# Optimization experiments

Hardware: AMD Instinct MI355X
Metric: run time of the kernel (lower is better)

The kernel has to match this reference:

```python
import jax, jax.numpy as jnp
import numpy as np

N_HEADS = 16
HEAD_DIM = 128


def _rotate_half(x):
    x1, x2 = jnp.split(x, 2, axis=-1)
    return jnp.concatenate((-x2, x1), axis=-1)


def setup_inputs() -> dict:
    key = jax.random.key(0)
    ks = jax.random.split(key, 6)
    B, T, D = 2, 2048, 2048
    d = D // N_HEADS  # 128
    x = jax.random.normal(ks[0], (B, T, D), dtype=jnp.float32)
    # RoPE tables (shape [1,1,T,head_dim]) built as in standard implementations
    inv_freq = 1.0 / (10000.0 ** (jnp.arange(0, d, 2, dtype=jnp.float32) / d))
    ang = jnp.arange(T, dtype=jnp.float32)[:, None] * inv_freq[None, :]  # [T, d/2]
    emb = jnp.concatenate((ang, ang), axis=-1)  # [T, d]
    rope_cos = jnp.cos(emb)[None, None]
    rope_sin = jnp.sin(emb)[None, None]
    qkv_w = jax.random.normal(ks[1], (3 * D, D), dtype=jnp.float32) * (1.0 / np.sqrt(D))
    qkv_b = jnp.zeros((3 * D,), dtype=jnp.float32)
    out_w = jax.random.normal(ks[2], (D, D), dtype=jnp.float32) * (1.0 / np.sqrt(D))
    out_b = jnp.zeros((D,), dtype=jnp.float32)
    return {"x": x, "rope_cos": rope_cos, "rope_sin": rope_sin,
            "qkv_w": qkv_w, "qkv_b": qkv_b, "out_w": out_w, "out_b": out_b}


def reference(x, rope_cos, rope_sin, qkv_w, qkv_b, out_w, out_b):
    B, T, D = x.shape
    H, d = N_HEADS, D // N_HEADS
    # fused QKV projection: [B,T,3D] -> [3,B,H,T,d]
    qkv = (jnp.einsum('btd,ed->bte', x, qkv_w) + qkv_b)
    qkv = qkv.reshape(B, T, 3, H, d).transpose(2, 0, 3, 1, 4)
    q, k, v = qkv[0], qkv[1], qkv[2]
    cos = rope_cos[:, :, :T, :].astype(q.dtype)
    sin = rope_sin[:, :, :T, :].astype(q.dtype)
    q = q * cos + _rotate_half(q) * sin
    k = k * cos + _rotate_half(k) * sin
    # causal SDPA
    scale = 1.0 / jnp.sqrt(jnp.array(d, dtype=q.dtype))
    scores = jnp.einsum('bhqd,bhkd->bhqk', q, k) * scale  # [B,H,T,T]
    causal = jnp.tril(jnp.ones((T, T), dtype=bool))
    scores = jnp.where(causal, scores, jnp.finfo(scores.dtype).min)
    attn = jax.nn.softmax(scores, axis=-1)
    out = jnp.einsum('bhqk,bhkd->bhqd', attn, v)  # [B,H,T,d]
    out = out.transpose(0, 2, 1, 3).reshape(B, T, D)
    return jnp.einsum('btd,ed->bte', out, out_w) + out_b
```

## Files before the change

kernel.cpp:

```cpp
#include <hip/hip_runtime.h>
#include <cstdint>
#include <cstddef>

typedef unsigned short u16;
using bf16x8 = __attribute__((ext_vector_type(8))) short;
using f32x4  = __attribute__((ext_vector_type(4))) float;

#define MFMA16(a, b, c) __builtin_amdgcn_mfma_f32_16x16x32_bf16((a), (b), (c), 0, 0, 0)

__device__ __forceinline__ u16 f2bf(float f) {
  union { float f; unsigned u; } x; x.f = f;
  unsigned r = x.u + 0x7fffu + ((x.u >> 16) & 1u);
  return (u16)(r >> 16);
}
__device__ __forceinline__ float bf2f(u16 h) {
  union { unsigned u; float f; } x; x.u = ((unsigned)h) << 16;
  return x.f;
}
__device__ __forceinline__ void gll16(const void* g, void* l) {
  __builtin_amdgcn_global_load_lds((const __attribute__((address_space(1))) void*)g,
                                   (__attribute__((address_space(3))) void*)l, 16, 0, 0);
}

union U8 { bf16x8 v; u16 u[8]; };

__global__ __launch_bounds__(256) void cvt_kernel(const float* __restrict__ in,
                                                  u16* __restrict__ out, int n4) {
  int i = blockIdx.x * blockDim.x + threadIdx.x;
  if (i >= n4) return;
  float4 v = ((const float4*)in)[i];
  ushort4 o;
  o.x = f2bf(v.x); o.y = f2bf(v.y); o.z = f2bf(v.z); o.w = f2bf(v.w);
  ((ushort4*)out)[i] = o;
}

__global__ __launch_bounds__(512, 2) void gemm_bt256(const u16* __restrict__ A,
                                                     const u16* __restrict__ Bw,
                                                     const float* __restrict__ bias,
                                                     void* __restrict__ Cout,
                                                     int M, int N, int K, int out_bf16) {
  __shared__ u16 As_[2][16384];
  __shared__ u16 Bs_[2][16384];
  const int tid = threadIdx.x;
  const int lane = tid & 63, wave = tid >> 6;
  const int col = lane & 15, quad = lane >> 4;
  const int wr = wave >> 2, wc = wave & 3;
  const int bm = blockIdx.y, bn = blockIdx.x;
  const u16* Ag = A + (size_t)bm * 256 * K;
  const u16* Bg = Bw + (size_t)bn * 256 * K;
  const int srow = tid >> 2;
  const int sslot = tid & 3;
  const int ssw = (sslot ^ ((srow >> 1) & 3)) << 3;
  const size_t g0 = (size_t)srow * K + ssw;
  const size_t g1 = (size_t)(srow + 128) * K + ssw;
  const int swq = (quad ^ ((col >> 1) & 3)) << 3;
  const int aro = (wr * 128 + col) * 32 + swq;
  const int bro = (wc * 64 + col) * 32 + swq;
  u16* const As0 = &As_[0][0]; u16* const As1 = &As_[1][0];
  u16* const Bs0 = &Bs_[0][0]; u16* const Bs1 = &Bs_[1][0];
  f32x4 acc[8][4] = {};
  bf16x8 a[8], bq[2];
  const int NI = K >> 7;

#define STG_A(BUF, KS, KT) do { \
    gll16(Ag + g0 + (KT) + (KS) * 32, (void*)((BUF) + (KS) * 8192 + tid * 8)); \
    gll16(Ag + g1 + (KT) + (KS) * 32, (void*)((BUF) + (KS) * 8192 + 4096 + tid * 8)); } while (0)
#define STG_B(BUF, KS, KT) do { \
    gll16(Bg + g0 + (KT) + (KS) * 32, (void*)((BUF) + (KS) * 8192 + tid * 8)); \
    gll16(Bg + g1 + (KT) + (KS) * 32, (void*)((BUF) + (KS) * 8192 + 4096 + tid * 8)); } while (0)
#define RD_A(BUF, KS) do { _Pragma("unroll") \
    for (int m_ = 0; m_ < 8; m_++) \
      a[m_] = *(const bf16x8*)&(BUF)[(KS) * 8192 + aro + m_ * 512]; } while (0)
#define RD_B(BUF, KS, NH) do { _Pragma("unroll") \
    for (int n_ = 0; n_ < 2; n_++) \
      bq[n_] = *(const bf16x8*)&(BUF)[(KS) * 8192 + bro + ((NH) * 2 + n_) * 512]; } while (0)
#define MM(NH) do { _Pragma("unroll") \
    for (int m_ = 0; m_ < 8; m_++) { _Pragma("unroll") \
      for (int n_ = 0; n_ < 2; n_++) \
        acc[m_][(NH) * 2 + n_] = MFMA16(a[m_], bq[n_], acc[m_][(NH) * 2 + n_]); } } while (0)
#define PH(RDS, STGS, MMS, WT) do { \
    RDS; STGS; \
    __builtin_amdgcn_s_barrier(); \
    asm volatile("s_waitcnt lgkmcnt(0)" ::: "memory"); \
    __builtin_amdgcn_s_setprio(1); \
    MMS; \
    __builtin_amdgcn_s_setprio(0); \
    WT; \
    __builtin_amdgcn_s_barrier(); } while (0)
#define VM6 do { asm volatile("s_waitcnt vmcnt(6)" ::: "memory"); } while (0)
#define VM0 do { asm volatile("s_waitcnt vmcnt(0)" ::: "memory"); } while (0)
#define NOPW do { } while (0)

#define ITER(I, LAST) do { \
    const int kt1_ = ((2 * (I) + 1) << 6), kt2_ = kt1_ + 64, kt3_ = kt2_ + 64; \
    PH({ RD_A(As0, 0); RD_B(Bs0, 0, 0); }, { STG_B(Bs1, 1, kt1_); },                MM(0), NOPW); \
    PH({ RD_B(Bs0, 0, 1); },               { if (!(LAST)) STG_A(As0, 0, kt2_); },   MM(1), NOPW); \
    PH({ RD_A(As0, 1); RD_B(Bs0, 1, 1); }, { if (!(LAST)) STG_B(Bs0, 0, kt2_); },   MM(1), NOPW); \
    PH({ RD_B(Bs0, 1, 0); },               { if (!(LAST)) STG_A(As0, 1, kt2_); },   MM(0), \
       if (LAST) { VM0; } else { VM6; }); \
    PH({ RD_A(As1, 0); RD_B(Bs1, 0, 0); }, { if (!(LAST)) STG_B(Bs0, 1, kt2_); },   MM(0), NOPW); \
    PH({ RD_B(Bs1, 0, 1); },               { if (!(LAST)) STG_A(As1, 0, kt3_); },   MM(1), NOPW); \
    PH({ RD_A(As1, 1); RD_B(Bs1, 1, 1); }, { if (!(LAST)) STG_B(Bs1, 0, kt3_); },   MM(1), NOPW); \
    PH({ RD_B(Bs1, 1, 0); },               { if (!(LAST)) STG_A(As1, 1, kt3_); },   MM(0), \
       if (!(LAST)) { VM6; }); \
  } while (0)

  STG_A(As0, 0, 0);  STG_B(Bs0, 0, 0);  STG_A(As0, 1, 0);  STG_B(Bs0, 1, 0);
  STG_A(As1, 0, 64); STG_B(Bs1, 0, 64); STG_A(As1, 1, 64);
  VM6;
  __builtin_amdgcn_s_barrier();

  for (int i = 0; i < NI - 1; ++i) ITER(i, false);
  ITER(NI - 1, true);

#pragma unroll
  for (int i = 0; i < 8; i++) {
    const int row0 = bm * 256 + wr * 128 + i * 16 + quad * 4;
#pragma unroll
    for (int j = 0; j < 4; j++) {
      const int cn = bn * 256 + wc * 64 + j * 16 + col;
      const float bv = bias[cn];
#pragma unroll
      for (int r = 0; r < 4; r++) {
        float v = acc[i][j][r] + bv;
        size_t off = (size_t)(row0 + r) * N + cn;
        if (out_bf16) ((u16*)Cout)[off] = f2bf(v);
        else          ((float*)Cout)[off] = v;
      }
    }
  }
#undef STG_A
#undef STG_B
#undef RD_A
#undef RD_B
#undef MM
#undef PH
#undef VM6
#undef VM0
#undef NOPW
#undef ITER
}

__global__ __launch_bounds__(256) void rope_kernel(const u16* __restrict__ qkv,
                                                   const float* __restrict__ cosT,
                                                   const float* __restrict__ sinT,
                                                   u16* __restrict__ qo,
                                                   u16* __restrict__ ko,
                                                   u16* __restrict__ vt) {
  __shared__ u16 vs[128 * 72];
  const int bh = blockIdx.x;
  const int b = bh >> 4, h = bh & 15;
  const int tb = blockIdx.y;
  const int tid = threadIdx.x;
  const int tl = tid >> 2;
  const int g = tid & 3;
  const int t = tb * 64 + tl;
  const size_t qrow = ((size_t)(b * 2048 + t)) * 6144 + h * 128;
  const size_t orow = ((size_t)bh * 2048 + t) * 128;
  const int tt = t * 128;
  const int dl = g * 16, dh = 64 + dl;
  const float scale = 0.08838834764831845f;
#pragma unroll
  for (int cch = 0; cch < 2; cch++) {
    const int o8 = cch * 8;
    U8 ql, qh, kl, kh, vl, vh;
    ql.v = *(const bf16x8*)&qkv[qrow + dl + o8];
    qh.v = *(const bf16x8*)&qkv[qrow + dh + o8];
    kl.v = *(const bf16x8*)&qkv[qrow + 2048 + dl + o8];
    kh.v = *(const bf16x8*)&qkv[qrow + 2048 + dh + o8];
    vl.v = *(const bf16x8*)&qkv[qrow + 4096 + dl + o8];
    vh.v = *(const bf16x8*)&qkv[qrow + 4096 + dh + o8];
    float cl[8], ch_[8], sl[8], sh_[8];
    *(float4*)&cl[0]  = *(const float4*)&cosT[tt + dl + o8];
    *(float4*)&cl[4]  = *(const float4*)&cosT[tt + dl + o8 + 4];
    *(float4*)&ch_[0] = *(const float4*)&cosT[tt + dh + o8];
    *(float4*)&ch_[4] = *(const float4*)&cosT[tt + dh + o8 + 4];
    *(float4*)&sl[0]  = *(const float4*)&sinT[tt + dl + o8];
    *(float4*)&sl[4]  = *(const float4*)&sinT[tt + dl + o8 + 4];
    *(float4*)&sh_[0] = *(const float4*)&sinT[tt + dh + o8];
    *(float4*)&sh_[4] = *(const float4*)&sinT[tt + dh + o8 + 4];
    U8 aq, bq, ak, bk;
#pragma unroll
    for (int i = 0; i < 8; i++) {
      float qlf = bf2f(ql.u[i]), qhf = bf2f(qh.u[i]);
      float klf = bf2f(kl.u[i]), khf = bf2f(kh.u[i]);
      aq.u[i] = f2bf((qlf * cl[i]  - qhf * sl[i])  * scale);
      bq.u[i] = f2bf((qhf * ch_[i] + qlf * sh_[i]) * scale);
      ak.u[i] = f2bf(klf * cl[i]  - khf * sl[i]);
      bk.u[i] = f2bf(khf * ch_[i] + klf * sh_[i]);
    }
    *(bf16x8*)&qo[orow + dl + o8] = aq.v;
    *(bf16x8*)&qo[orow + dh + o8] = bq.v;
    *(bf16x8*)&ko[orow + dl + o8] = ak.v;
    *(bf16x8*)&ko[orow + dh + o8] = bk.v;
#pragma unroll
    for (int i = 0; i < 8; i++) {
      vs[(dl + o8 + i) * 72 + tl] = vl.u[i];
      vs[(dh + o8 + i) * 72 + tl] = vh.u[i];
    }
  }
  __syncthreads();
#pragma unroll
  for (int c = 0; c < 4; c++) {
    int idx = c * 256 + tid;
    int dd = idx >> 3, chk = idx & 7;
    bf16x8 vv = *(const bf16x8*)&vs[dd * 72 + chk * 8];
    *(bf16x8*)&vt[((size_t)bh * 128 + dd) * 2048 + tb * 64 + chk * 8] = vv;
  }
}

__global__ __launch_bounds__(256) void attn_kernel(const u16* __restrict__ Q,
                                                   const u16* __restrict__ Kk,
                                                   const u16* __restrict__ Vt,
                                                   u16* __restrict__ O) {
  __shared__ u16 Ks[64 * 136];
  __shared__ u16 Vs[128 * 72];
  __shared__ u16 Ps[4][16 * 72];
  const int bh = blockIdx.y, b = bh >> 4, h = bh & 15;
  const int qtile = gridDim.x - 1 - blockIdx.x;
  const int qb = qtile * 128;
  const int tid = threadIdx.x, wave = tid >> 6, lane = tid & 63;
  const int col = lane & 15, quad = lane >> 4;
  const int qw0 = qb + wave * 32;
  const int qw1 = qw0 + 16;
  const u16* Qg = Q + (size_t)bh * 2048 * 128;
  const u16* Kg = Kk + (size_t)bh * 2048 * 128;
  const u16* Vg = Vt + (size_t)bh * 128 * 2048;
  bf16x8 qf0[4], qf1[4];
#pragma unroll
  for (int c = 0; c < 4; c++) {
    qf0[c] = *(const bf16x8*)&Qg[(size_t)(qw0 + col) * 128 + c * 32 + quad * 8];
    qf1[c] = *(const bf16x8*)&Qg[(size_t)(qw1 + col) * 128 + c * 32 + quad * 8];
  }
  f32x4 o0[8] = {}, o1[8] = {};
  float ls0[4] = {0.f, 0.f, 0.f, 0.f}, ls1[4] = {0.f, 0.f, 0.f, 0.f};
  const int ntiles = (qb + 128) >> 6;
  const int kr = tid >> 2, kc = (tid & 3) * 8;
  const int vr = tid >> 1, vc = (tid & 1) * 8;
  for (int it = 0; it < ntiles; ++it) {
    const int kt = it << 6;
    __syncthreads();
#pragma unroll
    for (int u = 0; u < 4; u++)
      *(bf16x8*)&Ks[kr * 136 + kc + u * 32] =
          *(const bf16x8*)&Kg[(size_t)(kt + kr) * 128 + kc + u * 32];
#pragma unroll
    for (int u = 0; u < 4; u++)
      *(bf16x8*)&Vs[vr * 72 + vc + u * 16] =
          *(const bf16x8*)&Vg[(size_t)vr * 2048 + kt + vc + u * 16];
    __syncthreads();
    if (kt > qw1 + 15) continue;
    const bool do0 = (kt <= qw0 + 15);
    f32x4 s0[4] = {}, s1[4] = {};
#pragma unroll
    for (int c = 0; c < 4; c++) {
#pragma unroll
      for (int kg = 0; kg < 4; kg++) {
        bf16x8 kf = *(const bf16x8*)&Ks[(kg * 16 + col) * 136 + c * 32 + quad * 8];
        s0[kg] = MFMA16(qf0[c], kf, s0[kg]);
        s1[kg] = MFMA16(qf1[c], kf, s1[kg]);
      }
    }
    u16* pw = Ps[wave];
    if (do0) {
#pragma unroll
      for (int kg = 0; kg < 4; kg++)
#pragma unroll
        for (int r = 0; r < 4; r++) {
          int key = kt + kg * 16 + col, qg = qw0 + quad * 4 + r;
          float p = (key <= qg) ? __expf(s0[kg][r]) : 0.f;
          ls0[r] += p;
          pw[(quad * 4 + r) * 72 + kg * 16 + col] = f2bf(p);
        }
#pragma unroll
      for (int ks = 0; ks < 64; ks += 32) {
        bf16x8 pf = *(const bf16x8*)&pw[col * 72 + ks + quad * 8];
#pragma unroll
        for (int dt = 0; dt < 8; dt++) {
          bf16x8 vf = *(const bf16x8*)&Vs[(dt * 16 + col) * 72 + ks + quad * 8];
          o0[dt] = MFMA16(pf, vf, o0[dt]);
        }
      }
    }
    {
#pragma unroll
      for (int kg = 0; kg < 4; kg++)
#pragma unroll
        for (int r = 0; r < 4; r++) {
          int key = kt + kg * 16 + col, qg = qw1 + quad * 4 + r;
          float p = (key <= qg) ? __expf(s1[kg][r]) : 0.f;
          ls1[r] += p;
          pw[(quad * 4 + r) * 72 + kg * 16 + col] = f2bf(p);
        }
#pragma unroll
      for (int ks = 0; ks < 64; ks += 32) {
        bf16x8 pf = *(const bf16x8*)&pw[col * 72 + ks + quad * 8];
#pragma unroll
        for (int dt = 0; dt < 8; dt++) {
          bf16x8 vf = *(const bf16x8*)&Vs[(dt * 16 + col) * 72 + ks + quad * 8];
          o1[dt] = MFMA16(pf, vf, o1[dt]);
        }
      }
    }
  }
#pragma unroll
  for (int st = 1; st < 16; st <<= 1)
#pragma unroll
    for (int r = 0; r < 4; r++) {
      ls0[r] += __shfl_xor(ls0[r], st);
      ls1[r] += __shfl_xor(ls1[r], st);
    }
#pragma unroll
  for (int r = 0; r < 4; r++) {
    float inv0 = 1.0f / ls0[r], inv1 = 1.0f / ls1[r];
    size_t row0 = ((size_t)(b * 2048 + qw0 + quad * 4 + r)) * 2048 + h * 128;
    size_t row1 = ((size_t)(b * 2048 + qw1 + quad * 4 + r)) * 2048 + h * 128;
#pragma unroll
    for (int dt = 0; dt < 8; dt++) {
      O[row0 + dt * 16 + col] = f2bf(o0[dt][r] * inv0);
      O[row1 + dt * 16 + col] = f2bf(o1[dt][r] * inv1);
    }
  }
}

extern "C" void kernel_launch(void* const* d_in, const int* in_sizes, int n_in,
                              void* d_out, int out_size, void* d_ws, size_t ws_size,
                              hipStream_t stream) {
  const float* x        = (const float*)d_in[0];
  const float* rope_cos = (const float*)d_in[1];
  const float* rope_sin = (const float*)d_in[2];
  const float* qkv_w    = (const float*)d_in[3];
  const float* qkv_b    = (const float*)d_in[4];
  const float* out_w    = (const float*)d_in[5];
  const float* out_b    = (const float*)d_in[6];
  float* out = (float*)d_out;
  u16* ws = (u16*)d_ws;
  u16* xb    = ws;
  u16* wqkvb = xb + 8388608;
  u16* woutb = wqkvb + 12582912;
  u16* qkvb  = woutb + 4194304;
  u16* qb    = qkvb + 25165824;
  u16* kb    = qb + 8388608;
  u16* vtb   = kb + 8388608;
  u16* attnb = xb;

  cvt_kernel<<<8192, 256, 0, stream>>>(x, xb, 2097152);
  cvt_kernel<<<12288, 256, 0, stream>>>(qkv_w, wqkvb, 3145728);
  cvt_kernel<<<4096, 256, 0, stream>>>(out_w, woutb, 1048576);
  gemm_bt256<<<dim3(24, 16), 512, 0, stream>>>(xb, wqkvb, qkv_b, qkvb, 4096, 6144, 2048, 1);
  rope_kernel<<<dim3(32, 32), 256, 0, stream>>>(qkvb, rope_cos, rope_sin, qb, kb, vtb);
  attn_kernel<<<dim3(16, 32), 256, 0, stream>>>(qb, kb, vtb, attnb);
  gemm_bt256<<<dim3(8, 16), 512, 0, stream>>>(attnb, woutb, out_b, out, 4096, 2048, 2048, 0);
}
```

Baseline: 452.4 us.

## Add triple-buffered NT GEMM for output projection and swizzle attention LDS tiles

Adds a templated gemm_nt kernel with a 256x128 tile, triple-buffered global-to-LDS loads, split MFMA phases with priority hints and an XOR-swizzled LDS layout. It is used for the output projection so that the grid is 256 blocks instead of 128, giving better CU coverage. The attention kernel also replaces its padded K/V shared-memory layouts with XOR-swizzled unpadded ones to cut bank conflicts and LDS footprint. The new GEMM's vmcnt accounting has to stay correct for the 2-column-tile variant; if it does not, the results are wrong.

```diff
diff --git a/kernel.cpp b/kernel.cpp
--- a/kernel.cpp
+++ b/kernel.cpp
@@ -141,6 +141,105 @@
 #undef ITER
 }
 
+template<int NBF>
+__global__ __launch_bounds__(512, 2) void gemm_nt(const u16* __restrict__ A,
+                                                  const u16* __restrict__ Bw,
+                                                  const float* __restrict__ bias,
+                                                  void* __restrict__ Cout,
+                                                  int M, int N, int K, int out_bf16) {
+  __shared__ u16 As[3][8192];
+  __shared__ u16 Bs[3][NBF * 2048];
+  const int tid = threadIdx.x;
+  const int lane = tid & 63, wave = tid >> 6;
+  const int col = lane & 15, quad = lane >> 4;
+  const int wr = wave >> 2, wc = wave & 3;
+  const int bm = blockIdx.y, bn = blockIdx.x;
+  const u16* Ag = A + (size_t)bm * 256 * K;
+  const u16* Bg = Bw + (size_t)bn * (NBF * 64) * K;
+  const int srow = tid >> 2;
+  const int ssw = ((tid & 3) ^ ((srow >> 1) & 3)) << 3;
+  const size_t ga0 = (size_t)srow * K + ssw;
+  const size_t ga1 = (size_t)(srow + 128) * K + ssw;
+  const int swq = (quad ^ ((col >> 1) & 3)) << 3;
+  const int aro = (wr * 128 + col) * 32 + swq;
+  const int bro = (wc * (NBF * 16) + col) * 32 + swq;
+  f32x4 acc[8][NBF] = {};
+  const int NT = K >> 5;
+
+#define STG_A(BI, KT) do { \
+    gll16(Ag + ga0 + (KT), (void*)(&As[BI][0] + tid * 8)); \
+    gll16(Ag + ga1 + (KT), (void*)(&As[BI][0] + 4096 + tid * 8)); } while (0)
+#define STG_B(BI, KT) do { \
+    gll16(Bg + ga0 + (KT), (void*)(&Bs[BI][0] + tid * 8)); \
+    if (NBF == 4) gll16(Bg + ga1 + (KT), (void*)(&Bs[BI][0] + 4096 + tid * 8)); } while (0)
+
+  STG_A(0, 0); STG_B(0, 0); STG_A(1, 32); STG_B(1, 32);
+  if (NBF == 4) asm volatile("s_waitcnt vmcnt(4)" ::: "memory");
+  else          asm volatile("s_waitcnt vmcnt(3)" ::: "memory");
+  __builtin_amdgcn_s_barrier();
+
+  int cA = 0, cB = 1, cC = 2;
+  for (int t = 0; t < NT; ++t) {
+    const u16* Ab = &As[cA][0];
+    const u16* Bb = &Bs[cA][0];
+    const bool pf = (t + 2) < NT;
+    const int k2 = (t + 2) << 5;
+    bf16x8 a1[4], a2[4], b[NBF];
+#pragma unroll
+    for (int j = 0; j < 4; j++) a1[j] = *(const bf16x8*)&Ab[aro + j * 512];
+#pragma unroll
+    for (int n = 0; n < NBF; n++) b[n] = *(const bf16x8*)&Bb[bro + n * 512];
+    if (pf) STG_A(cC, k2);
+    __builtin_amdgcn_s_barrier();
+    __builtin_amdgcn_s_setprio(1);
+#pragma unroll
+    for (int m = 0; m < 4; m++)
+#pragma unroll
+      for (int n = 0; n < NBF; n++)
+        acc[m][n] = MFMA16(a1[m], b[n], acc[m][n]);
+    __builtin_amdgcn_s_setprio(0);
+    __builtin_amdgcn_s_barrier();
+#pragma unroll
+    for (int j = 0; j < 4; j++) a2[j] = *(const bf16x8*)&Ab[aro + (4 + j) * 512];
+    if (pf) STG_B(cC, k2);
+    __builtin_amdgcn_s_barrier();
+    __builtin_amdgcn_s_setprio(1);
+#pragma unroll
+    for (int m = 0; m < 4; m++)
+#pragma unroll
+      for (int n = 0; n < NBF; n++)
+        acc[4 + m][n] = MFMA16(a2[m], b[n], acc[4 + m][n]);
+    __builtin_amdgcn_s_setprio(0);
+    if (pf) {
+      if (NBF == 4) asm volatile("s_waitcnt vmcnt(4)" ::: "memory");
+      else          asm volatile("s_waitcnt vmcnt(3)" ::: "memory");
+    } else {
+      asm volatile("s_waitcnt vmcnt(0)" ::: "memory");
+    }
+    __builtin_amdgcn_s_barrier();
+    int tmp = cA; cA = cB; cB = cC; cC = tmp;
+  }
+
+#pragma unroll
+  for (int i = 0; i < 8; i++) {
+    const int row0 = bm * 256 + wr * 128 + i * 16 + quad * 4;
+#pragma unroll
+    for (int j = 0; j < NBF; j++) {
+      const int cn = bn * (NBF * 64) + wc * (NBF * 16) + j * 16 + col;
+      const float bv = bias[cn];
+#pragma unroll
+      for (int r = 0; r < 4; r++) {
+        float v = acc[i][j][r] + bv;
+        size_t off = (size_t)(row0 + r) * N + cn;
+        if (out_bf16) ((u16*)Cout)[off] = f2bf(v);
+        else          ((float*)Cout)[off] = v;
+      }
+    }
+  }
+#undef STG_A
+#undef STG_B
+}
+
 __global__ __launch_bounds__(256) void rope_kernel(const u16* __restrict__ qkv,
                                                    const float* __restrict__ cosT,
                                                    const float* __restrict__ sinT,
@@ -213,8 +312,8 @@
                                                    const u16* __restrict__ Kk,
                                                    const u16* __restrict__ Vt,
                                                    u16* __restrict__ O) {
-  __shared__ u16 Ks[64 * 136];
-  __shared__ u16 Vs[128 * 72];
+  __shared__ u16 Ks[64 * 128];
+  __shared__ u16 Vs[128 * 64];
   __shared__ u16 Ps[4][16 * 72];
   const int bh = blockIdx.y, b = bh >> 4, h = bh & 15;
   const int qtile = gridDim.x - 1 - blockIdx.x;
@@ -235,19 +334,23 @@
   f32x4 o0[8] = {}, o1[8] = {};
   float ls0[4] = {0.f, 0.f, 0.f, 0.f}, ls1[4] = {0.f, 0.f, 0.f, 0.f};
   const int ntiles = (qb + 128) >> 6;
-  const int kr = tid >> 2, kc = (tid & 3) * 8;
-  const int vr = tid >> 1, vc = (tid & 1) * 8;
+  const int skr = tid >> 4, sks = tid & 15;
+  const int svr = tid >> 1, svc = tid & 1;
   for (int it = 0; it < ntiles; ++it) {
     const int kt = it << 6;
     __syncthreads();
 #pragma unroll
-    for (int u = 0; u < 4; u++)
-      *(bf16x8*)&Ks[kr * 136 + kc + u * 32] =
-          *(const bf16x8*)&Kg[(size_t)(kt + kr) * 128 + kc + u * 32];
-#pragma unroll
-    for (int u = 0; u < 4; u++)
-      *(bf16x8*)&Vs[vr * 72 + vc + u * 16] =
-          *(const bf16x8*)&Vg[(size_t)vr * 2048 + kt + vc + u * 16];
+    for (int u = 0; u < 4; u++) {
+      const int row = u * 16 + skr;
+      *(bf16x8*)&Ks[row * 128 + ((sks ^ (row & 7)) << 3)] =
+          *(const bf16x8*)&Kg[(size_t)(kt + row) * 128 + (sks << 3)];
+    }
+#pragma unroll
+    for (int u = 0; u < 4; u++) {
+      const int ch = svc + 2 * u;
+      *(bf16x8*)&Vs[svr * 64 + ((ch ^ (svr & 7)) << 3)] =
+          *(const bf16x8*)&Vg[(size_t)svr * 2048 + kt + (ch << 3)];
+    }
     __syncthreads();
     if (kt > qw1 + 15) continue;
     const bool do0 = (kt <= qw0 + 15);
@@ -256,7 +359,8 @@
     for (int c = 0; c < 4; c++) {
 #pragma unroll
       for (int kg = 0; kg < 4; kg++) {
-        bf16x8 kf = *(const bf16x8*)&Ks[(kg * 16 + col) * 136 + c * 32 + quad * 8];
+        const int krow = kg * 16 + col;
+        bf16x8 kf = *(const bf16x8*)&Ks[krow * 128 + (((c * 4 + quad) ^ (krow & 7)) << 3)];
         s0[kg] = MFMA16(qf0[c], kf, s0[kg]);
         s1[kg] = MFMA16(qf1[c], kf, s1[kg]);
       }
@@ -277,7 +381,8 @@
         bf16x8 pf = *(const bf16x8*)&pw[col * 72 + ks + quad * 8];
 #pragma unroll
         for (int dt = 0; dt < 8; dt++) {
-          bf16x8 vf = *(const bf16x8*)&Vs[(dt * 16 + col) * 72 + ks + quad * 8];
+          const int vrow = dt * 16 + col;
+          bf16x8 vf = *(const bf16x8*)&Vs[vrow * 64 + ((((ks >> 3) + quad) ^ (vrow & 7)) << 3)];
           o0[dt] = MFMA16(pf, vf, o0[dt]);
         }
       }
@@ -297,7 +402,8 @@
         bf16x8 pf = *(const bf16x8*)&pw[col * 72 + ks + quad * 8];
 #pragma unroll
         for (int dt = 0; dt < 8; dt++) {
-          bf16x8 vf = *(const bf16x8*)&Vs[(dt * 16 + col) * 72 + ks + quad * 8];
+          const int vrow = dt * 16 + col;
+          bf16x8 vf = *(const bf16x8*)&Vs[vrow * 64 + ((((ks >> 3) + quad) ^ (vrow & 7)) << 3)];
           o1[dt] = MFMA16(pf, vf, o1[dt]);
         }
       }
@@ -350,5 +456,5 @@
   gemm_bt256<<<dim3(24, 16), 512, 0, stream>>>(xb, wqkvb, qkv_b, qkvb, 4096, 6144, 2048, 1);
   rope_kernel<<<dim3(32, 32), 256, 0, stream>>>(qkvb, rope_cos, rope_sin, qb, kb, vtb);
   attn_kernel<<<dim3(16, 32), 256, 0, stream>>>(qb, kb, vtb, attnb);
-  gemm_bt256<<<dim3(8, 16), 512, 0, stream>>>(attnb, woutb, out_b, out, 4096, 2048, 2048, 0);
-}
+  gemm_nt<2><<<dim3(16, 16), 512, 0, stream>>>(attnb, woutb, out_b, out, 4096, 2048, 2048, 0);
+}
```

Result: slower. 505.3 us (+11.7%).

## Double-buffer K/V tiles with async global_load_lds and XOR-swizzled LDS layout

Applied to the files above, without the earlier changes.

Replaces the synchronous register-staged K/V tile loads in the attention kernel with direct global-to-LDS loads into two buffers, so the next tile is prefetched while the current one is computed. It also switches the K, V and P shared-memory tiles from padded layouts to XOR-swizzled layouts to avoid bank conflicts. This roughly doubles LDS use per block, which can lower occupancy. It also relies on manual vmcnt waits and raw barriers being correct.

```diff
diff --git a/kernel.cpp b/kernel.cpp
--- a/kernel.cpp
+++ b/kernel.cpp
@@ -213,9 +213,9 @@
                                                    const u16* __restrict__ Kk,
                                                    const u16* __restrict__ Vt,
                                                    u16* __restrict__ O) {
-  __shared__ u16 Ks[64 * 136];
-  __shared__ u16 Vs[128 * 72];
-  __shared__ u16 Ps[4][16 * 72];
+  __shared__ u16 Ks[2][8192];
+  __shared__ u16 Vs[2][8192];
+  __shared__ u16 Ps[4][1024];
   const int bh = blockIdx.y, b = bh >> 4, h = bh & 15;
   const int qtile = gridDim.x - 1 - blockIdx.x;
   const int qb = qtile * 128;
@@ -235,74 +235,102 @@
   f32x4 o0[8] = {}, o1[8] = {};
   float ls0[4] = {0.f, 0.f, 0.f, 0.f}, ls1[4] = {0.f, 0.f, 0.f, 0.f};
   const int ntiles = (qb + 128) >> 6;
-  const int kr = tid >> 2, kc = (tid & 3) * 8;
-  const int vr = tid >> 1, vc = (tid & 1) * 8;
+
+#define STAGE(IT, BUF) do { \
+    const int kt_ = (IT) << 6; \
+    _Pragma("unroll") \
+    for (int u_ = 0; u_ < 4; u_++) { \
+      const int ch_ = u_ * 256 + tid; \
+      const int kr_ = ch_ >> 4, s_ = ch_ & 15; \
+      gll16(Kg + (size_t)(kt_ + kr_) * 128 + ((s_ ^ (kr_ & 7)) << 3), \
+            (void*)(&Ks[BUF][0] + ch_ * 8)); \
+    } \
+    _Pragma("unroll") \
+    for (int u_ = 0; u_ < 4; u_++) { \
+      const int ch_ = u_ * 256 + tid; \
+      const int vr_ = ch_ >> 3, c_ = ch_ & 7; \
+      gll16(Vg + (size_t)vr_ * 2048 + kt_ + ((c_ ^ (vr_ & 7)) << 3), \
+            (void*)(&Vs[BUF][0] + ch_ * 8)); \
+    } \
+  } while (0)
+
+  STAGE(0, 0);
   for (int it = 0; it < ntiles; ++it) {
     const int kt = it << 6;
-    __syncthreads();
-#pragma unroll
-    for (int u = 0; u < 4; u++)
-      *(bf16x8*)&Ks[kr * 136 + kc + u * 32] =
-          *(const bf16x8*)&Kg[(size_t)(kt + kr) * 128 + kc + u * 32];
-#pragma unroll
-    for (int u = 0; u < 4; u++)
-      *(bf16x8*)&Vs[vr * 72 + vc + u * 16] =
-          *(const bf16x8*)&Vg[(size_t)vr * 2048 + kt + vc + u * 16];
-    __syncthreads();
-    if (kt > qw1 + 15) continue;
-    const bool do0 = (kt <= qw0 + 15);
-    f32x4 s0[4] = {}, s1[4] = {};
-#pragma unroll
-    for (int c = 0; c < 4; c++) {
-#pragma unroll
-      for (int kg = 0; kg < 4; kg++) {
-        bf16x8 kf = *(const bf16x8*)&Ks[(kg * 16 + col) * 136 + c * 32 + quad * 8];
-        s0[kg] = MFMA16(qf0[c], kf, s0[kg]);
-        s1[kg] = MFMA16(qf1[c], kf, s1[kg]);
-      }
-    }
-    u16* pw = Ps[wave];
-    if (do0) {
-#pragma unroll
-      for (int kg = 0; kg < 4; kg++)
-#pragma unroll
-        for (int r = 0; r < 4; r++) {
-          int key = kt + kg * 16 + col, qg = qw0 + quad * 4 + r;
-          float p = (key <= qg) ? __expf(s0[kg][r]) : 0.f;
-          ls0[r] += p;
-          pw[(quad * 4 + r) * 72 + kg * 16 + col] = f2bf(p);
-        }
-#pragma unroll
-      for (int ks = 0; ks < 64; ks += 32) {
-        bf16x8 pf = *(const bf16x8*)&pw[col * 72 + ks + quad * 8];
-#pragma unroll
-        for (int dt = 0; dt < 8; dt++) {
-          bf16x8 vf = *(const bf16x8*)&Vs[(dt * 16 + col) * 72 + ks + quad * 8];
-          o0[dt] = MFMA16(pf, vf, o0[dt]);
+    const int cur = it & 1;
+    if (it + 1 < ntiles) {
+      STAGE(it + 1, (it + 1) & 1);
+      asm volatile("s_waitcnt vmcnt(8)" ::: "memory");
+    } else {
+      asm volatile("s_waitcnt vmcnt(0)" ::: "memory");
+    }
+    __builtin_amdgcn_s_barrier();
+    if (kt <= qw1 + 15) {
+      const bool do0 = (kt <= qw0 + 15);
+      const u16* Kb = &Ks[cur][0];
+      const u16* Vb = &Vs[cur][0];
+      f32x4 s0[4] = {}, s1[4] = {};
+#pragma unroll
+      for (int c = 0; c < 4; c++) {
+#pragma unroll
+        for (int kg = 0; kg < 4; kg++) {
+          const int krow = kg * 16 + col;
+          bf16x8 kf = *(const bf16x8*)&Kb[krow * 128 + (((c * 4 + quad) ^ (krow & 7)) << 3)];
+          s0[kg] = MFMA16(qf0[c], kf, s0[kg]);
+          s1[kg] = MFMA16(qf1[c], kf, s1[kg]);
         }
       }
-    }
-    {
-#pragma unroll
-      for (int kg = 0; kg < 4; kg++)
-#pragma unroll
-        for (int r = 0; r < 4; r++) {
-          int key = kt + kg * 16 + col, qg = qw1 + quad * 4 + r;
-          float p = (key <= qg) ? __expf(s1[kg][r]) : 0.f;
-          ls1[r] += p;
-          pw[(quad * 4 + r) * 72 + kg * 16 + col] = f2bf(p);
-        }
-#pragma unroll
-      for (int ks = 0; ks < 64; ks += 32) {
-        bf16x8 pf = *(const bf16x8*)&pw[col * 72 + ks + quad * 8];
-#pragma unroll
-        for (int dt = 0; dt < 8; dt++) {
-          bf16x8 vf = *(const bf16x8*)&Vs[(dt * 16 + col) * 72 + ks + quad * 8];
-          o1[dt] = MFMA16(pf, vf, o1[dt]);
+      u16* pw = Ps[wave];
+      if (do0) {
+#pragma unroll
+        for (int kg = 0; kg < 4; kg++)
+#pragma unroll
+          for (int r = 0; r < 4; r++) {
+            int key = kt + kg * 16 + col, qg = qw0 + quad * 4 + r;
+            float p = (key <= qg) ? __expf(s0[kg][r]) : 0.f;
+            ls0[r] += p;
+            const int prow = quad * 4 + r;
+            pw[prow * 64 + (((kg * 2 + (col >> 3)) ^ (prow & 7)) << 3) + (col & 7)] = f2bf(p);
+          }
+#pragma unroll
+        for (int ks = 0; ks < 64; ks += 32) {
+          bf16x8 pf = *(const bf16x8*)&pw[col * 64 + ((((ks >> 3) + quad) ^ (col & 7)) << 3)];
+#pragma unroll
+          for (int dt = 0; dt < 8; dt++) {
+            const int vrow = dt * 16 + col;
+            bf16x8 vf = *(const bf16x8*)&Vb[vrow * 64 + ((((ks >> 3) + quad) ^ (vrow & 7)) << 3)];
+            o0[dt] = MFMA16(pf, vf, o0[dt]);
+          }
         }
       }
-    }
-  }
+      {
+#pragma unroll
+        for (int kg = 0; kg < 4; kg++)
+#pragma unroll
+          for (int r = 0; r < 4; r++) {
+            int key = kt + kg * 16 + col, qg = qw1 + quad * 4 + r;
+            float p = (key <= qg) ? __expf(s1[kg][r]) : 0.f;
+            ls1[r] += p;
+            const int prow = quad * 4 + r;
+            pw[prow * 64 + (((kg * 2 + (col >> 3)) ^ (prow & 7)) << 3) + (col & 7)] = f2bf(p);
+          }
+#pragma unroll
+        for (int ks = 0; ks < 64; ks += 32) {
+          bf16x8 pf = *(const bf16x8*)&pw[col * 64 + ((((ks >> 3) + quad) ^ (col & 7)) << 3)];
+#pragma unroll
+          for (int dt = 0; dt < 8; dt++) {
+            const int vrow = dt * 16 + col;
+            bf16x8 vf = *(const bf16x8*)&Vb[vrow * 64 + ((((ks >> 3) + quad) ^ (vrow & 7)) << 3)];
+            o1[dt] = MFMA16(pf, vf, o1[dt]);
+          }
+        }
+      }
+    }
+    asm volatile("" ::: "memory");
+    __builtin_amdgcn_s_barrier();
+  }
+#undef STAGE
+
 #pragma unroll
   for (int st = 1; st < 16; st <<= 1)
 #pragma unroll
```

Measured after the change: 508.0 us. +12.3%, slower.
